# Kernel optimization log

Hardware: AMD Instinct MI355X
Metric: run time of the kernel (lower is better)

## Reference

```python
import jax, jax.numpy as jnp
import numpy as np

INF = 1e10  # stand-in for the original global INF constant
D_MODEL = 1024
N_HEADS = 16
SCALE = float(np.sqrt(D_MODEL))  # Attention is built with full d_key, so scale = sqrt(d_model)


def setup_inputs() -> dict:
    key = jax.random.key(0)
    ks = jax.random.split(key, 8)
    B, S, D = 4, 2048, D_MODEL
    s = 1.0 / np.sqrt(D)
    return {
        "query": jax.random.normal(ks[0], (B, S, D), jnp.float32),
        "key": jax.random.normal(ks[1], (B, S, D), jnp.float32),
        "value": jax.random.normal(ks[2], (B, S, D), jnp.float32),
        "wq": jax.random.normal(ks[3], (D, D), jnp.float32) * s,
        "bq": jnp.zeros((D,), jnp.float32),
        "wk": jax.random.normal(ks[4], (D, D), jnp.float32) * s,
        "bk": jnp.zeros((D,), jnp.float32),
        "wv": jax.random.normal(ks[5], (D, D), jnp.float32) * s,
        "bv": jnp.zeros((D,), jnp.float32),
        "wo": jax.random.normal(ks[6], (D, D), jnp.float32) * s,
        "bo": jnp.zeros((D,), jnp.float32),
    }


def reference(query, key, value, wq, bq, wk, bk, wv, bv, wo, bo):
    B, S, D = query.shape
    H = N_HEADS
    dh = D // H
    q = query @ wq + bq
    k = key @ wk + bk
    v = value @ wv + bv
    # split heads: [B, S, H, dh]
    q = q.reshape(B, S, H, dh)
    k = k.reshape(B, S, H, dh)
    v = v.reshape(B, S, H, dh)
    # raw dot products (unscaled), then causal mask subtracted (as in original),
    # then divide by sqrt(d_key) and softmax
    scores = jnp.einsum("bqhd,bkhd->bhqk", q, k)
    causal = jnp.triu(jnp.ones((S, S), scores.dtype), k=1) * INF
    scores = scores - causal  # broadcast over [B, H]
    attn = jax.nn.softmax(scores / SCALE, axis=-1)
    out = jnp.einsum("bhqk,bkhd->bqhd", attn, v).reshape(B, S, D)
    return out @ wo + bo
```

## Files before the change

kernel.cpp:

```cpp
#include <hip/hip_runtime.h>
#include <hip/hip_bf16.h>

typedef __bf16 bf16_t;
typedef __bf16 bf16x8 __attribute__((ext_vector_type(8)));
typedef float f32x4 __attribute__((ext_vector_type(4)));

#define MFMA16(a, b, c) __builtin_amdgcn_mfma_f32_16x16x32_bf16((a), (b), (c), 0, 0, 0)

static constexpr int S_LEN = 2048;
static constexpr int DM = 1024;
static constexpr int NH = 16;
static constexpr int DH = 64;

typedef const __attribute__((address_space(1))) unsigned int gu32;
typedef __attribute__((address_space(3))) unsigned int lu32;
__device__ __forceinline__ void gl_lds16(const void* src, void* dst) {
    __builtin_amdgcn_global_load_lds((gu32*)src, (lu32*)dst, 16, 0, 0);
}

struct PreArgs { const float* w[4]; bf16_t* o[4]; const float* s[3]; bf16_t* d[3]; };

__global__ __launch_bounds__(256) void pre_kernel(PreArgs p) {
    int bid = blockIdx.x;
    int tid = threadIdx.x;
    if (bid < 1024) {
        int wi = bid >> 8;
        int tb = bid & 255;
        int k0 = (tb >> 4) * 64;
        int n0 = (tb & 15) * 64;
        const float* w = p.w[wi];
        bf16_t* o = p.o[wi];
        __shared__ bf16_t t[64 * 66];
#pragma unroll
        for (int i = 0; i < 4; ++i) {
            int f = tid + 256 * i;
            int row = f >> 4;
            int c4 = f & 15;
            f32x4 v = *reinterpret_cast<const f32x4*>(w + (size_t)(k0 + row) * DM + n0 + c4 * 4);
            int base = row * 66 + c4 * 4;
            t[base + 0] = (bf16_t)v[0];
            t[base + 1] = (bf16_t)v[1];
            t[base + 2] = (bf16_t)v[2];
            t[base + 3] = (bf16_t)v[3];
        }
        __syncthreads();
#pragma unroll
        for (int i = 0; i < 2; ++i) {
            int c = tid + 256 * i;
            int n = c >> 3;
            int ck = c & 7;
            union { bf16_t h[8]; uint4 u; } cv;
#pragma unroll
            for (int j = 0; j < 8; ++j) cv.h[j] = t[(ck * 8 + j) * 66 + n];
            *reinterpret_cast<uint4*>(o + (size_t)(n0 + n) * DM + k0 + ck * 8) = cv.u;
        }
    } else {
        int cbid = bid - 1024;
        int ti = cbid >> 12;
        size_t idx = (size_t)(((cbid & 4095) << 8) | tid) * 8;
        const float* s = p.s[ti];
        bf16_t* d = p.d[ti];
        f32x4 v0 = *reinterpret_cast<const f32x4*>(s + idx);
        f32x4 v1 = *reinterpret_cast<const f32x4*>(s + idx + 4);
        union { bf16_t h[8]; uint4 u; } cv;
#pragma unroll
        for (int j = 0; j < 4; ++j) { cv.h[j] = (bf16_t)v0[j]; cv.h[4 + j] = (bf16_t)v1[j]; }
        *reinterpret_cast<uint4*>(d + idx) = cv.u;
    }
}

template <int MODE>
__global__ __launch_bounds__(256) void gemm_k(const bf16_t* __restrict__ Ab,
                                              const bf16_t* __restrict__ BT,
                                              const float* __restrict__ bias,
                                              void* __restrict__ Cp, float alpha) {
    constexpr int K = 1024, N = 1024;
    int bid = blockIdx.x;
    int bm = (bid & 7) * 8 + ((bid >> 3) & 7);
    int bn = bid >> 6;
    int tid = threadIdx.x;
    int w = tid >> 6, l = tid & 63;
    int g = l >> 4, lc = l & 15;

    __shared__ bf16_t a_buf[2][128 * 32];
    __shared__ bf16_t b_buf[2][128 * 32];

    f32x4 zero = {0.f, 0.f, 0.f, 0.f};
    f32x4 acc[4][4];
#pragma unroll
    for (int m = 0; m < 4; ++m)
#pragma unroll
        for (int n = 0; n < 4; ++n) acc[m][n] = zero;

    int m0 = bm * 128, n0 = bn * 128;
    int wr = (w >> 1) * 64, wc = (w & 1) * 64;

    auto stage = [&](int buf, int kt) {
        int k0 = kt * 32;
#pragma unroll
        for (int i = 0; i < 2; ++i) {
            int r16 = (w * 2 + i) * 16;
            int row = r16 + (l >> 2), ch = l & 3;
            gl_lds16(Ab + (size_t)(m0 + row) * K + k0 + ch * 8, &a_buf[buf][r16 * 32]);
            gl_lds16(BT + (size_t)(n0 + row) * K + k0 + ch * 8, &b_buf[buf][r16 * 32]);
        }
    };

    stage(0, 0);
    int cur = 0;
    for (int kt = 0; kt < K / 32; ++kt) {
        __syncthreads();
        if (kt + 1 < K / 32) stage(cur ^ 1, kt + 1);
        bf16x8 af[4], bfr[4];
#pragma unroll
        for (int m = 0; m < 4; ++m)
            af[m] = *reinterpret_cast<bf16x8*>(&a_buf[cur][(wr + m * 16 + lc) * 32 + g * 8]);
#pragma unroll
        for (int n = 0; n < 4; ++n)
            bfr[n] = *reinterpret_cast<bf16x8*>(&b_buf[cur][(wc + n * 16 + lc) * 32 + g * 8]);
#pragma unroll
        for (int m = 0; m < 4; ++m)
#pragma unroll
            for (int n = 0; n < 4; ++n)
                acc[m][n] = MFMA16(af[m], bfr[n], acc[m][n]);
        cur ^= 1;
    }

    if constexpr (MODE == 2) {
#pragma unroll
        for (int n = 0; n < 4; ++n) {
            int ng = n0 + wc + n * 16 + lc;
            float bv = bias[ng];
            int h = ng >> 6, d = ng & 63;
#pragma unroll
            for (int m = 0; m < 4; ++m) {
                int s0g = m0 + wr + m * 16 + g * 4;
                int b = s0g >> 11, s0 = s0g & 2047;
                union { bf16_t hh[4]; uint2 u; } pk;
#pragma unroll
                for (int r = 0; r < 4; ++r)
                    pk.hh[r] = (bf16_t)((acc[m][n][r] + bv) * alpha);
                *reinterpret_cast<uint2*>(
                    &((bf16_t*)Cp)[(((size_t)(b * NH + h)) * DH + d) * S_LEN + s0]) = pk.u;
            }
        }
    } else {
#pragma unroll
        for (int n = 0; n < 4; ++n) {
            int ng = n0 + wc + n * 16 + lc;
            float bv = bias[ng];
#pragma unroll
            for (int m = 0; m < 4; ++m) {
#pragma unroll
                for (int r = 0; r < 4; ++r) {
                    int mg = m0 + wr + m * 16 + g * 4 + r;
                    float v = (acc[m][n][r] + bv) * alpha;
                    if constexpr (MODE == 0) {
                        int b = mg >> 11, s = mg & 2047, h = ng >> 6, d = ng & 63;
                        ((bf16_t*)Cp)[(((size_t)(b * NH + h)) * S_LEN + s) * DH + d] = (bf16_t)v;
                    } else {
                        ((float*)Cp)[(size_t)mg * N + ng] = v;
                    }
                }
            }
        }
    }
}

__global__ __launch_bounds__(256) void attn_kernel(const bf16_t* __restrict__ Qh,
                                                   const bf16_t* __restrict__ Kh,
                                                   const bf16_t* __restrict__ Vt,
                                                   bf16_t* __restrict__ AO) {
    int bid = blockIdx.x;
    int qt = 31 - (bid >> 6);
    int bh = bid & 63;
    int h = bh & 15;
    int b = bh >> 4;
    int tid = threadIdx.x;
    int w = tid >> 6, l = tid & 63;
    int g = l >> 4, lc = l & 15;
    int q0 = qt * 64 + w * 16;
    int q = q0 + lc;

    __shared__ bf16_t k_lds[2][64 * 64];
    __shared__ bf16_t v_lds[2][64 * 64];
    __shared__ bf16_t p_lds[4][16 * 64];

    size_t head_off = ((size_t)(b * NH + h)) * S_LEN * DH;
    const bf16_t* Kp = Kh + head_off;
    const bf16_t* Vp = Vt + head_off;

    bf16x8 qf[2];
    {
        const bf16_t* qp = Qh + head_off + (size_t)(q0 + lc) * DH + g * 8;
        qf[0] = *reinterpret_cast<const bf16x8*>(qp);
        qf[1] = *reinterpret_cast<const bf16x8*>(qp + 32);
    }

    f32x4 zero = {0.f, 0.f, 0.f, 0.f};
    f32x4 o_acc[4];
#pragma unroll
    for (int nt = 0; nt < 4; ++nt) o_acc[nt] = zero;
    float l_part = 0.f;

    int sw = lc & 7;

    auto stageKV = [&](int buf, int kv0) {
#pragma unroll
        for (int i = 0; i < 2; ++i) {
            int r8 = w * 16 + i * 8;
            int row = r8 + (l >> 3);
            int sc_ = (l & 7) ^ (row & 7);
            gl_lds16(Kp + (size_t)(kv0 + row) * DH + sc_ * 8, &k_lds[buf][r8 * 64]);
            gl_lds16(Vp + (size_t)row * S_LEN + kv0 + sc_ * 8, &v_lds[buf][r8 * 64]);
        }
    };

    stageKV(0, 0);
    int cur = 0;
    for (int t = 0; t <= qt; ++t) {
        int kv0 = t * 64;
        __syncthreads();
        if (t < qt) stageKV(cur ^ 1, kv0 + 64);

        f32x4 sc[4];
#pragma unroll
        for (int nt = 0; nt < 4; ++nt) {
            int row = nt * 16 + lc;
            bf16x8 kf0 = *reinterpret_cast<bf16x8*>(&k_lds[cur][row * 64 + ((g) ^ sw) * 8]);
            bf16x8 kf1 = *reinterpret_cast<bf16x8*>(&k_lds[cur][row * 64 + ((4 + g) ^ sw) * 8]);
            f32x4 s = zero;
            s = MFMA16(kf0, qf[0], s);
            s = MFMA16(kf1, qf[1], s);
            sc[nt] = s;
        }
        if (t == qt) {
#pragma unroll
            for (int nt = 0; nt < 4; ++nt)
#pragma unroll
                for (int r = 0; r < 4; ++r) {
                    int kv = kv0 + nt * 16 + g * 4 + r;
                    if (kv > q) sc[nt][r] = -1e30f;
                }
        }
#pragma unroll
        for (int nt = 0; nt < 4; ++nt)
#pragma unroll
            for (int r = 0; r < 4; ++r) sc[nt][r] = exp2f(sc[nt][r]);
#pragma unroll
        for (int nt = 0; nt < 4; ++nt)
            l_part += sc[nt][0] + sc[nt][1] + sc[nt][2] + sc[nt][3];
#pragma unroll
        for (int nt = 0; nt < 4; ++nt) {
            union { bf16_t hh[4]; uint2 u; } pk;
#pragma unroll
            for (int r = 0; r < 4; ++r) pk.hh[r] = (bf16_t)sc[nt][r];
            int cu = nt * 2 + (g >> 1);
            *reinterpret_cast<uint2*>(
                &p_lds[w][lc * 64 + ((cu ^ sw) * 8) + (g & 1) * 4]) = pk.u;
        }
        bf16x8 pf0 = *reinterpret_cast<bf16x8*>(&p_lds[w][lc * 64 + ((g) ^ sw) * 8]);
        bf16x8 pf1 = *reinterpret_cast<bf16x8*>(&p_lds[w][lc * 64 + ((4 + g) ^ sw) * 8]);
#pragma unroll
        for (int nt = 0; nt < 4; ++nt) {
            int row = nt * 16 + lc;
            bf16x8 vf0 = *reinterpret_cast<bf16x8*>(&v_lds[cur][row * 64 + ((g) ^ sw) * 8]);
            bf16x8 vf1 = *reinterpret_cast<bf16x8*>(&v_lds[cur][row * 64 + ((4 + g) ^ sw) * 8]);
            o_acc[nt] = MFMA16(pf0, vf0, o_acc[nt]);
            o_acc[nt] = MFMA16(pf1, vf1, o_acc[nt]);
        }
        cur ^= 1;
    }

    float l_s = l_part;
    l_s += __shfl_xor(l_s, 16, 64);
    l_s += __shfl_xor(l_s, 32, 64);

#pragma unroll
    for (int r = 0; r < 4; ++r) {
        float lr = __shfl(l_s, g * 4 + r, 64);
        float inv = 1.0f / lr;
        int qq = q0 + g * 4 + r;
        size_t base = ((size_t)b * S_LEN + qq) * DM + h * DH;
#pragma unroll
        for (int nt = 0; nt < 4; ++nt)
            AO[base + nt * 16 + lc] = (bf16_t)(o_acc[nt][r] * inv);
    }
}

extern "C" void kernel_launch(void* const* d_in, const int* in_sizes, int n_in,
                              void* d_out, int out_size, void* d_ws, size_t ws_size,
                              hipStream_t stream) {
    (void)in_sizes; (void)n_in; (void)out_size; (void)ws_size;
    const float* query = (const float*)d_in[0];
    const float* key   = (const float*)d_in[1];
    const float* value = (const float*)d_in[2];
    const float* wq = (const float*)d_in[3];
    const float* bq = (const float*)d_in[4];
    const float* wk = (const float*)d_in[5];
    const float* bk = (const float*)d_in[6];
    const float* wv = (const float*)d_in[7];
    const float* bv = (const float*)d_in[8];
    const float* wo = (const float*)d_in[9];
    const float* bo = (const float*)d_in[10];
    float* out = (float*)d_out;

    char* ws = (char*)d_ws;
    const size_t Mi = (size_t)1 << 20;
    bf16_t* wqT = (bf16_t*)(ws + 0 * Mi);
    bf16_t* wkT = (bf16_t*)(ws + 2 * Mi);
    bf16_t* wvT = (bf16_t*)(ws + 4 * Mi);
    bf16_t* woT = (bf16_t*)(ws + 6 * Mi);
    bf16_t* Qh  = (bf16_t*)(ws + 8 * Mi);
    bf16_t* Kh  = (bf16_t*)(ws + 24 * Mi);
    bf16_t* Vt  = (bf16_t*)(ws + 40 * Mi);
    bf16_t* AO  = (bf16_t*)(ws + 56 * Mi);
    bf16_t* Xq  = (bf16_t*)(ws + 24 * Mi);
    bf16_t* Xk  = (bf16_t*)(ws + 40 * Mi);
    bf16_t* Xv  = (bf16_t*)(ws + 56 * Mi);

    PreArgs p;
    p.w[0] = wq; p.w[1] = wk; p.w[2] = wv; p.w[3] = wo;
    p.o[0] = wqT; p.o[1] = wkT; p.o[2] = wvT; p.o[3] = woT;
    p.s[0] = query; p.s[1] = key; p.s[2] = value;
    p.d[0] = Xq; p.d[1] = Xk; p.d[2] = Xv;
    pre_kernel<<<dim3(1024 + 3 * 4096), dim3(256), 0, stream>>>(p);

    gemm_k<0><<<dim3(512), dim3(256), 0, stream>>>(Xq, wqT, bq, (void*)Qh, 0.04508422f);
    gemm_k<0><<<dim3(512), dim3(256), 0, stream>>>(Xk, wkT, bk, (void*)Kh, 1.0f);
    gemm_k<2><<<dim3(512), dim3(256), 0, stream>>>(Xv, wvT, bv, (void*)Vt, 1.0f);

    attn_kernel<<<dim3(2048), dim3(256), 0, stream>>>(Qh, Kh, Vt, AO);

    gemm_k<1><<<dim3(512), dim3(256), 0, stream>>>(AO, woT, bo, (void*)out, 1.0f);
}
```

Before: 217.7 us.

## Batch QKV projections into one launch, narrow output GEMM tiles, precompute attention load pointers

When the workspace holds at least 120 MiB, the three Q/K/V projection GEMMs run as a single 1536-block launch. This fills the GPU better and removes two launch gaps, but the inputs have to move to separate workspace regions because their old slots alias the outputs. The output projection now uses 128x64 tiles, giving 1024 blocks for better occupancy and wave balance, at the cost of less reuse per tile. The attention kernel precomputes its K/V global load pointers and advances them by increment instead of recomputing addresses each iteration.

```diff
diff --git a/kernel.cpp b/kernel.cpp
--- a/kernel.cpp
+++ b/kernel.cpp
@@ -69,11 +69,155 @@
     }
 }
 
+#define GEMM_CORE(Ab_, BT_)                                                          \
+    __shared__ bf16_t a_buf[2][128 * 32];                                            \
+    __shared__ bf16_t b_buf[2][128 * 32];                                            \
+    f32x4 zero = {0.f, 0.f, 0.f, 0.f};                                               \
+    f32x4 acc[4][4];                                                                 \
+    _Pragma("unroll") for (int m = 0; m < 4; ++m)                                    \
+        _Pragma("unroll") for (int n = 0; n < 4; ++n) acc[m][n] = zero;              \
+    int wr = (w >> 1) * 64, wc = (w & 1) * 64;                                       \
+    auto stage = [&](int buf, int kt) {                                              \
+        int k0 = kt * 32;                                                            \
+        _Pragma("unroll") for (int i = 0; i < 2; ++i) {                              \
+            int r16 = (w * 2 + i) * 16;                                              \
+            int row = r16 + (l >> 2), ch = l & 3;                                    \
+            gl_lds16(Ab_ + (size_t)(m0 + row) * 1024 + k0 + ch * 8, &a_buf[buf][r16 * 32]); \
+            gl_lds16(BT_ + (size_t)(n0 + row) * 1024 + k0 + ch * 8, &b_buf[buf][r16 * 32]); \
+        }                                                                            \
+    };                                                                               \
+    stage(0, 0);                                                                     \
+    int cur = 0;                                                                     \
+    for (int kt = 0; kt < 32; ++kt) {                                                \
+        __syncthreads();                                                             \
+        if (kt + 1 < 32) stage(cur ^ 1, kt + 1);                                     \
+        bf16x8 af[4], bfr[4];                                                        \
+        _Pragma("unroll") for (int m = 0; m < 4; ++m)                                \
+            af[m] = *reinterpret_cast<bf16x8*>(&a_buf[cur][(wr + m * 16 + lc) * 32 + g * 8]); \
+        _Pragma("unroll") for (int n = 0; n < 4; ++n)                                \
+            bfr[n] = *reinterpret_cast<bf16x8*>(&b_buf[cur][(wc + n * 16 + lc) * 32 + g * 8]); \
+        _Pragma("unroll") for (int m = 0; m < 4; ++m)                                \
+            _Pragma("unroll") for (int n = 0; n < 4; ++n)                            \
+                acc[m][n] = MFMA16(af[m], bfr[n], acc[m][n]);                        \
+        cur ^= 1;                                                                    \
+    }
+
+struct QKVArgs {
+    const bf16_t* A[3]; const bf16_t* BT[3]; const float* bias[3];
+    bf16_t* out[3]; float alpha0;
+};
+
+__global__ __launch_bounds__(256) void gemm_qkv(QKVArgs a) {
+    int bid = blockIdx.x;
+    int wi = bid >> 9;
+    int sub = bid & 511;
+    int bm = (sub & 7) * 8 + ((sub >> 3) & 7);
+    int bn = sub >> 6;
+    int tid = threadIdx.x;
+    int w = tid >> 6, l = tid & 63;
+    int g = l >> 4, lc = l & 15;
+    int m0 = bm * 128, n0 = bn * 128;
+    const bf16_t* Ap = a.A[wi];
+    const bf16_t* Bp = a.BT[wi];
+    GEMM_CORE(Ap, Bp)
+
+    float alpha = (wi == 0) ? a.alpha0 : 1.0f;
+    const float* bias = a.bias[wi];
+    bf16_t* Cp = a.out[wi];
+    if (wi == 2) {
+#pragma unroll
+        for (int n = 0; n < 4; ++n) {
+            int ng = n0 + wc + n * 16 + lc;
+            float bv = bias[ng];
+            int h = ng >> 6, d = ng & 63;
+#pragma unroll
+            for (int m = 0; m < 4; ++m) {
+                int s0g = m0 + wr + m * 16 + g * 4;
+                int b = s0g >> 11, s0 = s0g & 2047;
+                union { bf16_t hh[4]; uint2 u; } pk;
+#pragma unroll
+                for (int r = 0; r < 4; ++r)
+                    pk.hh[r] = (bf16_t)(acc[m][n][r] + bv);
+                *reinterpret_cast<uint2*>(
+                    &Cp[(((size_t)(b * NH + h)) * DH + d) * S_LEN + s0]) = pk.u;
+            }
+        }
+    } else {
+#pragma unroll
+        for (int n = 0; n < 4; ++n) {
+            int ng = n0 + wc + n * 16 + lc;
+            float bv = bias[ng];
+            int h = ng >> 6, d = ng & 63;
+#pragma unroll
+            for (int m = 0; m < 4; ++m) {
+#pragma unroll
+                for (int r = 0; r < 4; ++r) {
+                    int mg = m0 + wr + m * 16 + g * 4 + r;
+                    int b = mg >> 11, s = mg & 2047;
+                    Cp[(((size_t)(b * NH + h)) * S_LEN + s) * DH + d] =
+                        (bf16_t)((acc[m][n][r] + bv) * alpha);
+                }
+            }
+        }
+    }
+}
+
 template <int MODE>
 __global__ __launch_bounds__(256) void gemm_k(const bf16_t* __restrict__ Ab,
                                               const bf16_t* __restrict__ BT,
                                               const float* __restrict__ bias,
-                                              void* __restrict__ Cp, float alpha) {
+                                              bf16_t* __restrict__ Cp, float alpha) {
+    int bid = blockIdx.x;
+    int bm = (bid & 7) * 8 + ((bid >> 3) & 7);
+    int bn = bid >> 6;
+    int tid = threadIdx.x;
+    int w = tid >> 6, l = tid & 63;
+    int g = l >> 4, lc = l & 15;
+    int m0 = bm * 128, n0 = bn * 128;
+    GEMM_CORE(Ab, BT)
+
+    if constexpr (MODE == 2) {
+#pragma unroll
+        for (int n = 0; n < 4; ++n) {
+            int ng = n0 + wc + n * 16 + lc;
+            float bv = bias[ng];
+            int h = ng >> 6, d = ng & 63;
+#pragma unroll
+            for (int m = 0; m < 4; ++m) {
+                int s0g = m0 + wr + m * 16 + g * 4;
+                int b = s0g >> 11, s0 = s0g & 2047;
+                union { bf16_t hh[4]; uint2 u; } pk;
+#pragma unroll
+                for (int r = 0; r < 4; ++r)
+                    pk.hh[r] = (bf16_t)((acc[m][n][r] + bv) * alpha);
+                *reinterpret_cast<uint2*>(
+                    &Cp[(((size_t)(b * NH + h)) * DH + d) * S_LEN + s0]) = pk.u;
+            }
+        }
+    } else {
+#pragma unroll
+        for (int n = 0; n < 4; ++n) {
+            int ng = n0 + wc + n * 16 + lc;
+            float bv = bias[ng];
+            int h = ng >> 6, d = ng & 63;
+#pragma unroll
+            for (int m = 0; m < 4; ++m) {
+#pragma unroll
+                for (int r = 0; r < 4; ++r) {
+                    int mg = m0 + wr + m * 16 + g * 4 + r;
+                    int b = mg >> 11, s = mg & 2047;
+                    Cp[(((size_t)(b * NH + h)) * S_LEN + s) * DH + d] =
+                        (bf16_t)((acc[m][n][r] + bv) * alpha);
+                }
+            }
+        }
+    }
+}
+
+__global__ __launch_bounds__(256) void gemm_o(const bf16_t* __restrict__ Ab,
+                                              const bf16_t* __restrict__ BT,
+                                              const float* __restrict__ bias,
+                                              float* __restrict__ Cp) {
     constexpr int K = 1024, N = 1024;
     int bid = blockIdx.x;
     int bm = (bid & 7) * 8 + ((bid >> 3) & 7);
@@ -83,17 +227,17 @@
     int g = l >> 4, lc = l & 15;
 
     __shared__ bf16_t a_buf[2][128 * 32];
-    __shared__ bf16_t b_buf[2][128 * 32];
+    __shared__ bf16_t b_buf[2][64 * 32];
 
     f32x4 zero = {0.f, 0.f, 0.f, 0.f};
-    f32x4 acc[4][4];
+    f32x4 acc[4][2];
 #pragma unroll
     for (int m = 0; m < 4; ++m)
 #pragma unroll
-        for (int n = 0; n < 4; ++n) acc[m][n] = zero;
-
-    int m0 = bm * 128, n0 = bn * 128;
-    int wr = (w >> 1) * 64, wc = (w & 1) * 64;
+        for (int n = 0; n < 2; ++n) acc[m][n] = zero;
+
+    int m0 = bm * 128, n0 = bn * 64;
+    int wr = (w >> 1) * 64, wc = (w & 1) * 32;
 
     auto stage = [&](int buf, int kt) {
         int k0 = kt * 32;
@@ -102,8 +246,10 @@
             int r16 = (w * 2 + i) * 16;
             int row = r16 + (l >> 2), ch = l & 3;
             gl_lds16(Ab + (size_t)(m0 + row) * K + k0 + ch * 8, &a_buf[buf][r16 * 32]);
-            gl_lds16(BT + (size_t)(n0 + row) * K + k0 + ch * 8, &b_buf[buf][r16 * 32]);
-        }
+        }
+        int r16 = w * 16;
+        int row = r16 + (l >> 2), ch = l & 3;
+        gl_lds16(BT + (size_t)(n0 + row) * K + k0 + ch * 8, &b_buf[buf][r16 * 32]);
     };
 
     stage(0, 0);
@@ -111,57 +257,31 @@
     for (int kt = 0; kt < K / 32; ++kt) {
         __syncthreads();
         if (kt + 1 < K / 32) stage(cur ^ 1, kt + 1);
-        bf16x8 af[4], bfr[4];
+        bf16x8 af[4], bfr[2];
 #pragma unroll
         for (int m = 0; m < 4; ++m)
             af[m] = *reinterpret_cast<bf16x8*>(&a_buf[cur][(wr + m * 16 + lc) * 32 + g * 8]);
 #pragma unroll
-        for (int n = 0; n < 4; ++n)
+        for (int n = 0; n < 2; ++n)
             bfr[n] = *reinterpret_cast<bf16x8*>(&b_buf[cur][(wc + n * 16 + lc) * 32 + g * 8]);
 #pragma unroll
         for (int m = 0; m < 4; ++m)
 #pragma unroll
-            for (int n = 0; n < 4; ++n)
+            for (int n = 0; n < 2; ++n)
                 acc[m][n] = MFMA16(af[m], bfr[n], acc[m][n]);
         cur ^= 1;
     }
 
-    if constexpr (MODE == 2) {
-#pragma unroll
-        for (int n = 0; n < 4; ++n) {
-            int ng = n0 + wc + n * 16 + lc;
-            float bv = bias[ng];
-            int h = ng >> 6, d = ng & 63;
-#pragma unroll
-            for (int m = 0; m < 4; ++m) {
-                int s0g = m0 + wr + m * 16 + g * 4;
-                int b = s0g >> 11, s0 = s0g & 2047;
-                union { bf16_t hh[4]; uint2 u; } pk;
-#pragma unroll
-                for (int r = 0; r < 4; ++r)
-                    pk.hh[r] = (bf16_t)((acc[m][n][r] + bv) * alpha);
-                *reinterpret_cast<uint2*>(
-                    &((bf16_t*)Cp)[(((size_t)(b * NH + h)) * DH + d) * S_LEN + s0]) = pk.u;
-            }
-        }
-    } else {
-#pragma unroll
-        for (int n = 0; n < 4; ++n) {
-            int ng = n0 + wc + n * 16 + lc;
-            float bv = bias[ng];
-#pragma unroll
-            for (int m = 0; m < 4; ++m) {
-#pragma unroll
-                for (int r = 0; r < 4; ++r) {
-                    int mg = m0 + wr + m * 16 + g * 4 + r;
-                    float v = (acc[m][n][r] + bv) * alpha;
-                    if constexpr (MODE == 0) {
-                        int b = mg >> 11, s = mg & 2047, h = ng >> 6, d = ng & 63;
-                        ((bf16_t*)Cp)[(((size_t)(b * NH + h)) * S_LEN + s) * DH + d] = (bf16_t)v;
-                    } else {
-                        ((float*)Cp)[(size_t)mg * N + ng] = v;
-                    }
-                }
+#pragma unroll
+    for (int n = 0; n < 2; ++n) {
+        int ng = n0 + wc + n * 16 + lc;
+        float bv = bias[ng];
+#pragma unroll
+        for (int m = 0; m < 4; ++m) {
+#pragma unroll
+            for (int r = 0; r < 4; ++r) {
+                int mg = m0 + wr + m * 16 + g * 4 + r;
+                Cp[(size_t)mg * N + ng] = acc[m][n][r] + bv;
             }
         }
     }
@@ -187,8 +307,6 @@
     __shared__ bf16_t p_lds[4][16 * 64];
 
     size_t head_off = ((size_t)(b * NH + h)) * S_LEN * DH;
-    const bf16_t* Kp = Kh + head_off;
-    const bf16_t* Vp = Vt + head_off;
 
     bf16x8 qf[2];
     {
@@ -197,6 +315,19 @@
         qf[1] = *reinterpret_cast<const bf16x8*>(qp + 32);
     }
 
+    const bf16_t* kg0; const bf16_t* kg1; const bf16_t* vg0; const bf16_t* vg1;
+    int r8a = w * 16, r8b = w * 16 + 8;
+    {
+        const bf16_t* Kp = Kh + head_off;
+        const bf16_t* Vp = Vt + head_off;
+        int rowa = r8a + (l >> 3), rowb = r8b + (l >> 3);
+        int sca = (l & 7) ^ (rowa & 7), scb = (l & 7) ^ (rowb & 7);
+        kg0 = Kp + (size_t)rowa * DH + sca * 8;
+        kg1 = Kp + (size_t)rowb * DH + scb * 8;
+        vg0 = Vp + (size_t)rowa * S_LEN + sca * 8;
+        vg1 = Vp + (size_t)rowb * S_LEN + scb * 8;
+    }
+
     f32x4 zero = {0.f, 0.f, 0.f, 0.f};
     f32x4 o_acc[4];
 #pragma unroll
@@ -205,23 +336,22 @@
 
     int sw = lc & 7;
 
-    auto stageKV = [&](int buf, int kv0) {
-#pragma unroll
-        for (int i = 0; i < 2; ++i) {
-            int r8 = w * 16 + i * 8;
-            int row = r8 + (l >> 3);
-            int sc_ = (l & 7) ^ (row & 7);
-            gl_lds16(Kp + (size_t)(kv0 + row) * DH + sc_ * 8, &k_lds[buf][r8 * 64]);
-            gl_lds16(Vp + (size_t)row * S_LEN + kv0 + sc_ * 8, &v_lds[buf][r8 * 64]);
-        }
+    auto stageKV = [&](int buf) {
+        gl_lds16(kg0, &k_lds[buf][r8a * 64]);
+        gl_lds16(vg0, &v_lds[buf][r8a * 64]);
+        gl_lds16(kg1, &k_lds[buf][r8b * 64]);
+        gl_lds16(vg1, &v_lds[buf][r8b * 64]);
     };
 
-    stageKV(0, 0);
+    stageKV(0);
     int cur = 0;
     for (int t = 0; t <= qt; ++t) {
         int kv0 = t * 64;
         __syncthreads();
-        if (t < qt) stageKV(cur ^ 1, kv0 + 64);
+        if (t < qt) {
+            kg0 += 64 * DH; kg1 += 64 * DH; vg0 += 64; vg1 += 64;
+            stageKV(cur ^ 1);
+        }
 
         f32x4 sc[4];
 #pragma unroll
@@ -291,7 +421,7 @@
 extern "C" void kernel_launch(void* const* d_in, const int* in_sizes, int n_in,
                               void* d_out, int out_size, void* d_ws, size_t ws_size,
                               hipStream_t stream) {
-    (void)in_sizes; (void)n_in; (void)out_size; (void)ws_size;
+    (void)in_sizes; (void)n_in; (void)out_size;
     const float* query = (const float*)d_in[0];
     const float* key   = (const float*)d_in[1];
     const float* value = (const float*)d_in[2];
@@ -315,9 +445,22 @@
     bf16_t* Kh  = (bf16_t*)(ws + 24 * Mi);
     bf16_t* Vt  = (bf16_t*)(ws + 40 * Mi);
     bf16_t* AO  = (bf16_t*)(ws + 56 * Mi);
-    bf16_t* Xq  = (bf16_t*)(ws + 24 * Mi);
-    bf16_t* Xk  = (bf16_t*)(ws + 40 * Mi);
-    bf16_t* Xv  = (bf16_t*)(ws + 56 * Mi);
+
+    const float QALPHA = 0.04508422f;
+
+    bool fused = (ws_size >= 120 * Mi);
+    bf16_t* Xq;
+    bf16_t* Xk;
+    bf16_t* Xv;
+    if (fused) {
+        Xq = (bf16_t*)(ws + 72 * Mi);
+        Xk = (bf16_t*)(ws + 88 * Mi);
+        Xv = (bf16_t*)(ws + 104 * Mi);
+    } else {
+        Xq = (bf16_t*)(ws + 24 * Mi);
+        Xk = (bf16_t*)(ws + 40 * Mi);
+        Xv = (bf16_t*)(ws + 56 * Mi);
+    }
 
     PreArgs p;
     p.w[0] = wq; p.w[1] = wk; p.w[2] = wv; p.w[3] = wo;
@@ -326,11 +469,21 @@
     p.d[0] = Xq; p.d[1] = Xk; p.d[2] = Xv;
     pre_kernel<<<dim3(1024 + 3 * 4096), dim3(256), 0, stream>>>(p);
 
-    gemm_k<0><<<dim3(512), dim3(256), 0, stream>>>(Xq, wqT, bq, (void*)Qh, 0.04508422f);
-    gemm_k<0><<<dim3(512), dim3(256), 0, stream>>>(Xk, wkT, bk, (void*)Kh, 1.0f);
-    gemm_k<2><<<dim3(512), dim3(256), 0, stream>>>(Xv, wvT, bv, (void*)Vt, 1.0f);
+    if (fused) {
+        QKVArgs qa;
+        qa.A[0] = Xq; qa.A[1] = Xk; qa.A[2] = Xv;
+        qa.BT[0] = wqT; qa.BT[1] = wkT; qa.BT[2] = wvT;
+        qa.bias[0] = bq; qa.bias[1] = bk; qa.bias[2] = bv;
+        qa.out[0] = Qh; qa.out[1] = Kh; qa.out[2] = Vt;
+        qa.alpha0 = QALPHA;
+        gemm_qkv<<<dim3(1536), dim3(256), 0, stream>>>(qa);
+    } else {
+        gemm_k<0><<<dim3(512), dim3(256), 0, stream>>>(Xq, wqT, bq, Qh, QALPHA);
+        gemm_k<0><<<dim3(512), dim3(256), 0, stream>>>(Xk, wkT, bk, Kh, 1.0f);
+        gemm_k<2><<<dim3(512), dim3(256), 0, stream>>>(Xv, wvT, bv, Vt, 1.0f);
+    }
 
     attn_kernel<<<dim3(2048), dim3(256), 0, stream>>>(Qh, Kh, Vt, AO);
 
-    gemm_k<1><<<dim3(512), dim3(256), 0, stream>>>(AO, woT, bo, (void*)out, 1.0f);
-}
+    gemm_o<<<dim3(1024), dim3(256), 0, stream>>>(AO, woT, bo, out);
+}
```

Result: faster. 211.9 us (-2.7%).

## Use 128x64 GEMM tiles with LDS-staged coalesced epilogues and hoisted attention pointers

Applied to the files above, without the earlier changes.

Shrinks the GEMM tile from 128x128 to 128x64 and doubles the grid to 1024 blocks, so more CUs have work on this 8192x1024 problem. Stores for the head-split Q/K and transposed V outputs now go through an LDS buffer and are written as 16-byte coalesced chunks instead of scattered 2-byte writes. The attention kernel precomputes its K/V global pointers and advances them each iteration, which cuts address arithmetic. It also places the converted inputs in separate workspace regions when space allows. The cost is less reuse per tile and extra barriers in the epilogue.

```diff
diff --git a/kernel.cpp b/kernel.cpp
--- a/kernel.cpp
+++ b/kernel.cpp
@@ -70,11 +70,11 @@
 }
 
 template <int MODE>
-__global__ __launch_bounds__(256) void gemm_k(const bf16_t* __restrict__ Ab,
+__global__ __launch_bounds__(256) void gemm64(const bf16_t* __restrict__ Ab,
                                               const bf16_t* __restrict__ BT,
                                               const float* __restrict__ bias,
                                               void* __restrict__ Cp, float alpha) {
-    constexpr int K = 1024, N = 1024;
+    constexpr int K = 1024;
     int bid = blockIdx.x;
     int bm = (bid & 7) * 8 + ((bid >> 3) & 7);
     int bn = bid >> 6;
@@ -82,87 +82,121 @@
     int w = tid >> 6, l = tid & 63;
     int g = l >> 4, lc = l & 15;
 
-    __shared__ bf16_t a_buf[2][128 * 32];
-    __shared__ bf16_t b_buf[2][128 * 32];
+    __shared__ bf16_t smem[12288];
+    bf16_t* a_buf0 = smem;
+    bf16_t* a_buf1 = smem + 4096;
+    bf16_t* b_buf0 = smem + 8192;
+    bf16_t* b_buf1 = smem + 10240;
 
     f32x4 zero = {0.f, 0.f, 0.f, 0.f};
-    f32x4 acc[4][4];
+    f32x4 acc[4][2];
 #pragma unroll
     for (int m = 0; m < 4; ++m)
 #pragma unroll
-        for (int n = 0; n < 4; ++n) acc[m][n] = zero;
-
-    int m0 = bm * 128, n0 = bn * 128;
-    int wr = (w >> 1) * 64, wc = (w & 1) * 64;
-
-    auto stage = [&](int buf, int kt) {
+        for (int n = 0; n < 2; ++n) acc[m][n] = zero;
+
+    int m0 = bm * 128, n0 = bn * 64;
+    int wr = (w >> 1) * 64, wc = (w & 1) * 32;
+
+    auto stage = [&](bf16_t* ab, bf16_t* bb, int kt) {
         int k0 = kt * 32;
 #pragma unroll
         for (int i = 0; i < 2; ++i) {
             int r16 = (w * 2 + i) * 16;
             int row = r16 + (l >> 2), ch = l & 3;
-            gl_lds16(Ab + (size_t)(m0 + row) * K + k0 + ch * 8, &a_buf[buf][r16 * 32]);
-            gl_lds16(BT + (size_t)(n0 + row) * K + k0 + ch * 8, &b_buf[buf][r16 * 32]);
-        }
+            gl_lds16(Ab + (size_t)(m0 + row) * K + k0 + ch * 8, ab + r16 * 32);
+        }
+        int r16 = w * 16;
+        int row = r16 + (l >> 2), ch = l & 3;
+        gl_lds16(BT + (size_t)(n0 + row) * K + k0 + ch * 8, bb + r16 * 32);
     };
 
-    stage(0, 0);
+    stage(a_buf0, b_buf0, 0);
     int cur = 0;
     for (int kt = 0; kt < K / 32; ++kt) {
         __syncthreads();
-        if (kt + 1 < K / 32) stage(cur ^ 1, kt + 1);
-        bf16x8 af[4], bfr[4];
+        bf16_t* ab = cur ? a_buf1 : a_buf0;
+        bf16_t* bb = cur ? b_buf1 : b_buf0;
+        if (kt + 1 < K / 32) stage(cur ? a_buf0 : a_buf1, cur ? b_buf0 : b_buf1, kt + 1);
+        bf16x8 af[4], bfr[2];
 #pragma unroll
         for (int m = 0; m < 4; ++m)
-            af[m] = *reinterpret_cast<bf16x8*>(&a_buf[cur][(wr + m * 16 + lc) * 32 + g * 8]);
-#pragma unroll
-        for (int n = 0; n < 4; ++n)
-            bfr[n] = *reinterpret_cast<bf16x8*>(&b_buf[cur][(wc + n * 16 + lc) * 32 + g * 8]);
+            af[m] = *reinterpret_cast<bf16x8*>(&ab[(wr + m * 16 + lc) * 32 + g * 8]);
+#pragma unroll
+        for (int n = 0; n < 2; ++n)
+            bfr[n] = *reinterpret_cast<bf16x8*>(&bb[(wc + n * 16 + lc) * 32 + g * 8]);
 #pragma unroll
         for (int m = 0; m < 4; ++m)
 #pragma unroll
-            for (int n = 0; n < 4; ++n)
+            for (int n = 0; n < 2; ++n)
                 acc[m][n] = MFMA16(af[m], bfr[n], acc[m][n]);
         cur ^= 1;
     }
 
-    if constexpr (MODE == 2) {
-#pragma unroll
-        for (int n = 0; n < 4; ++n) {
+    if constexpr (MODE == 1) {
+        float* Cf = (float*)Cp;
+#pragma unroll
+        for (int n = 0; n < 2; ++n) {
             int ng = n0 + wc + n * 16 + lc;
             float bv = bias[ng];
-            int h = ng >> 6, d = ng & 63;
 #pragma unroll
             for (int m = 0; m < 4; ++m) {
-                int s0g = m0 + wr + m * 16 + g * 4;
-                int b = s0g >> 11, s0 = s0g & 2047;
+#pragma unroll
+                for (int r = 0; r < 4; ++r) {
+                    int mg = m0 + wr + m * 16 + g * 4 + r;
+                    Cf[(size_t)mg * 1024 + ng] = acc[m][n][r] + bv;
+                }
+            }
+        }
+    } else if constexpr (MODE == 0) {
+        __syncthreads();
+        bf16_t* eb = smem;
+#pragma unroll
+        for (int n = 0; n < 2; ++n) {
+            int d = wc + n * 16 + lc;
+            float bv = bias[n0 + d];
+#pragma unroll
+            for (int m = 0; m < 4; ++m)
+#pragma unroll
+                for (int r = 0; r < 4; ++r)
+                    eb[(wr + m * 16 + g * 4 + r) * 72 + d] =
+                        (bf16_t)((acc[m][n][r] + bv) * alpha);
+        }
+        __syncthreads();
+        int b = m0 >> 11, s0 = m0 & 2047, h = n0 >> 6;
+        bf16_t* dst = (bf16_t*)Cp + ((size_t)(b * NH + h) * S_LEN + s0) * DH;
+#pragma unroll
+        for (int p = 0; p < 4; ++p) {
+            int e = (p * 256 + tid) * 8;
+            int s = e >> 6, d = e & 63;
+            uint4 v = *reinterpret_cast<uint4*>(&eb[s * 72 + d]);
+            *reinterpret_cast<uint4*>(dst + e) = v;
+        }
+    } else {
+        __syncthreads();
+        bf16_t* eb = smem;
+#pragma unroll
+        for (int n = 0; n < 2; ++n) {
+            int d = wc + n * 16 + lc;
+            float bv = bias[n0 + d];
+#pragma unroll
+            for (int m = 0; m < 4; ++m) {
                 union { bf16_t hh[4]; uint2 u; } pk;
 #pragma unroll
                 for (int r = 0; r < 4; ++r)
                     pk.hh[r] = (bf16_t)((acc[m][n][r] + bv) * alpha);
-                *reinterpret_cast<uint2*>(
-                    &((bf16_t*)Cp)[(((size_t)(b * NH + h)) * DH + d) * S_LEN + s0]) = pk.u;
+                *reinterpret_cast<uint2*>(&eb[d * 136 + wr + m * 16 + g * 4]) = pk.u;
             }
         }
-    } else {
-#pragma unroll
-        for (int n = 0; n < 4; ++n) {
-            int ng = n0 + wc + n * 16 + lc;
-            float bv = bias[ng];
-#pragma unroll
-            for (int m = 0; m < 4; ++m) {
-#pragma unroll
-                for (int r = 0; r < 4; ++r) {
-                    int mg = m0 + wr + m * 16 + g * 4 + r;
-                    float v = (acc[m][n][r] + bv) * alpha;
-                    if constexpr (MODE == 0) {
-                        int b = mg >> 11, s = mg & 2047, h = ng >> 6, d = ng & 63;
-                        ((bf16_t*)Cp)[(((size_t)(b * NH + h)) * S_LEN + s) * DH + d] = (bf16_t)v;
-                    } else {
-                        ((float*)Cp)[(size_t)mg * N + ng] = v;
-                    }
-                }
-            }
+        __syncthreads();
+        int b = m0 >> 11, s0 = m0 & 2047, h = n0 >> 6;
+        bf16_t* dst = (bf16_t*)Cp + (size_t)(b * NH + h) * DH * S_LEN + s0;
+#pragma unroll
+        for (int p = 0; p < 4; ++p) {
+            int row = p * 16 + (tid >> 4);
+            int sc = (tid & 15) * 8;
+            uint4 v = *reinterpret_cast<uint4*>(&eb[row * 136 + sc]);
+            *reinterpret_cast<uint4*>(dst + (size_t)row * S_LEN + sc) = v;
         }
     }
 }
@@ -187,8 +221,6 @@
     __shared__ bf16_t p_lds[4][16 * 64];
 
     size_t head_off = ((size_t)(b * NH + h)) * S_LEN * DH;
-    const bf16_t* Kp = Kh + head_off;
-    const bf16_t* Vp = Vt + head_off;
 
     bf16x8 qf[2];
     {
@@ -197,6 +229,19 @@
         qf[1] = *reinterpret_cast<const bf16x8*>(qp + 32);
     }
 
+    const bf16_t* kg0; const bf16_t* kg1; const bf16_t* vg0; const bf16_t* vg1;
+    int r8a = w * 16, r8b = w * 16 + 8;
+    {
+        const bf16_t* Kp = Kh + head_off;
+        const bf16_t* Vp = Vt + head_off;
+        int rowa = r8a + (l >> 3), rowb = r8b + (l >> 3);
+        int sca = (l & 7) ^ (rowa & 7), scb = (l & 7) ^ (rowb & 7);
+        kg0 = Kp + (size_t)rowa * DH + sca * 8;
+        kg1 = Kp + (size_t)rowb * DH + scb * 8;
+        vg0 = Vp + (size_t)rowa * S_LEN + sca * 8;
+        vg1 = Vp + (size_t)rowb * S_LEN + scb * 8;
+    }
+
     f32x4 zero = {0.f, 0.f, 0.f, 0.f};
     f32x4 o_acc[4];
 #pragma unroll
@@ -205,23 +250,22 @@
 
     int sw = lc & 7;
 
-    auto stageKV = [&](int buf, int kv0) {
-#pragma unroll
-        for (int i = 0; i < 2; ++i) {
-            int r8 = w * 16 + i * 8;
-            int row = r8 + (l >> 3);
-            int sc_ = (l & 7) ^ (row & 7);
-            gl_lds16(Kp + (size_t)(kv0 + row) * DH + sc_ * 8, &k_lds[buf][r8 * 64]);
-            gl_lds16(Vp + (size_t)row * S_LEN + kv0 + sc_ * 8, &v_lds[buf][r8 * 64]);
-        }
+    auto stageKV = [&](int buf) {
+        gl_lds16(kg0, &k_lds[buf][r8a * 64]);
+        gl_lds16(vg0, &v_lds[buf][r8a * 64]);
+        gl_lds16(kg1, &k_lds[buf][r8b * 64]);
+        gl_lds16(vg1, &v_lds[buf][r8b * 64]);
     };
 
-    stageKV(0, 0);
+    stageKV(0);
     int cur = 0;
     for (int t = 0; t <= qt; ++t) {
         int kv0 = t * 64;
         __syncthreads();
-        if (t < qt) stageKV(cur ^ 1, kv0 + 64);
+        if (t < qt) {
+            kg0 += 64 * DH; kg1 += 64 * DH; vg0 += 64; vg1 += 64;
+            stageKV(cur ^ 1);
+        }
 
         f32x4 sc[4];
 #pragma unroll
@@ -291,7 +335,7 @@
 extern "C" void kernel_launch(void* const* d_in, const int* in_sizes, int n_in,
                               void* d_out, int out_size, void* d_ws, size_t ws_size,
                               hipStream_t stream) {
-    (void)in_sizes; (void)n_in; (void)out_size; (void)ws_size;
+    (void)in_sizes; (void)n_in; (void)out_size;
     const float* query = (const float*)d_in[0];
     const float* key   = (const float*)d_in[1];
     const float* value = (const float*)d_in[2];
@@ -315,9 +359,22 @@
     bf16_t* Kh  = (bf16_t*)(ws + 24 * Mi);
     bf16_t* Vt  = (bf16_t*)(ws + 40 * Mi);
     bf16_t* AO  = (bf16_t*)(ws + 56 * Mi);
-    bf16_t* Xq  = (bf16_t*)(ws + 24 * Mi);
-    bf16_t* Xk  = (bf16_t*)(ws + 40 * Mi);
-    bf16_t* Xv  = (bf16_t*)(ws + 56 * Mi);
+
+    const float QALPHA = 0.04508422f;
+
+    bool roomy = (ws_size >= 120 * Mi);
+    bf16_t* Xq;
+    bf16_t* Xk;
+    bf16_t* Xv;
+    if (roomy) {
+        Xq = (bf16_t*)(ws + 72 * Mi);
+        Xk = (bf16_t*)(ws + 88 * Mi);
+        Xv = (bf16_t*)(ws + 104 * Mi);
+    } else {
+        Xq = (bf16_t*)(ws + 24 * Mi);
+        Xk = (bf16_t*)(ws + 40 * Mi);
+        Xv = (bf16_t*)(ws + 56 * Mi);
+    }
 
     PreArgs p;
     p.w[0] = wq; p.w[1] = wk; p.w[2] = wv; p.w[3] = wo;
@@ -326,11 +383,11 @@
     p.d[0] = Xq; p.d[1] = Xk; p.d[2] = Xv;
     pre_kernel<<<dim3(1024 + 3 * 4096), dim3(256), 0, stream>>>(p);
 
-    gemm_k<0><<<dim3(512), dim3(256), 0, stream>>>(Xq, wqT, bq, (void*)Qh, 0.04508422f);
-    gemm_k<0><<<dim3(512), dim3(256), 0, stream>>>(Xk, wkT, bk, (void*)Kh, 1.0f);
-    gemm_k<2><<<dim3(512), dim3(256), 0, stream>>>(Xv, wvT, bv, (void*)Vt, 1.0f);
+    gemm64<0><<<dim3(1024), dim3(256), 0, stream>>>(Xq, wqT, bq, (void*)Qh, QALPHA);
+    gemm64<0><<<dim3(1024), dim3(256), 0, stream>>>(Xk, wkT, bk, (void*)Kh, 1.0f);
+    gemm64<2><<<dim3(1024), dim3(256), 0, stream>>>(Xv, wvT, bv, (void*)Vt, 1.0f);
 
     attn_kernel<<<dim3(2048), dim3(256), 0, stream>>>(Qh, Kh, Vt, AO);
 
-    gemm_k<1><<<dim3(512), dim3(256), 0, stream>>>(AO, woT, bo, (void*)out, 1.0f);
-}
+    gemm64<1><<<dim3(1024), dim3(256), 0, stream>>>(AO, woT, bo, (void*)out, 1.0f);
+}
```

Measured after the change: 218.7 us. No clear change (+0.4%).
